# Performance work log

Hardware: AMD Instinct MI355X
Metric: run time of the kernel (lower is better)

The kernel has to match this reference:

```python
import jax, jax.numpy as jnp
import numpy as np

N, E, G = 20000, 80000, 1000      # nodes, edges, graphs
F_TOT, EA = 16, 5                 # node feature dim, edge_attr dim
CSD = 5                           # cont_feat_start_dim
DIMS = [(5, 32), (32, 64), (64, 64)]  # NNConv (M_in, M_out) per layer
FC_IN = 64 + (F_TOT - CSD)        # 75


def setup_inputs() -> dict:
    key = jax.random.key(0)
    ks = iter(jax.random.split(key, 64))
    rnd = lambda sh: jax.random.normal(next(ks), sh, jnp.float32) * 0.1
    inp = {}
    inp["x"] = jax.random.normal(next(ks), (N, F_TOT), jnp.float32)
    inp["edge_index"] = jax.random.randint(next(ks), (2, E), 0, N)
    inp["edge_attr"] = jax.random.uniform(next(ks), (E, EA), dtype=jnp.float32)
    inp["batch"] = jnp.sort(jax.random.randint(next(ks), (N,), 0, G))
    for i, (mi, mo) in enumerate(DIMS, 1):
        inp[f"c{i}_w1"] = rnd((EA, 128))
        inp[f"c{i}_b1"] = jnp.zeros((128,), jnp.float32)
        inp[f"c{i}_w2"] = rnd((128, mi * mo))
        inp[f"c{i}_b2"] = jnp.zeros((mi * mo,), jnp.float32)
        inp[f"c{i}_root"] = rnd((mi, mo))
        inp[f"c{i}_bias"] = jnp.zeros((mo,), jnp.float32)
    inp["fc1_w"] = rnd((FC_IN, 32)); inp["fc1_b"] = jnp.zeros((32,), jnp.float32)
    inp["fc2_w"] = rnd((32, 16));    inp["fc2_b"] = jnp.zeros((16,), jnp.float32)
    inp["fc3_w"] = rnd((16, 1));     inp["fc3_b"] = jnp.zeros((1,), jnp.float32)
    return inp


def nnconv(h, edge_index, edge_attr, w1, b1, w2, b2, root, bias, mi, mo):
    # edge MLP -> per-edge [mi, mo] weight matrices
    hid = jax.nn.relu(edge_attr @ w1 + b1)                 # [E,128]
    W = (hid @ w2 + b2).reshape(-1, mi, mo)                # [E,mi,mo]
    src, dst = edge_index[0], edge_index[1]
    msg = jnp.einsum('ei,eio->eo', h[src], W)              # gather + per-edge matmul
    agg = jax.ops.segment_sum(msg, dst, num_segments=h.shape[0])  # scatter-add
    return agg + h @ root + bias


def reference(x, edge_index, edge_attr, batch,
              c1_w1, c1_b1, c1_w2, c1_b2, c1_root, c1_bias,
              c2_w1, c2_b1, c2_w2, c2_b2, c2_root, c2_bias,
              c3_w1, c3_b1, c3_w2, c3_b2, c3_root, c3_bias,
              fc1_w, fc1_b, fc2_w, fc2_b, fc3_w, fc3_b):
    convs = [(c1_w1, c1_b1, c1_w2, c1_b2, c1_root, c1_bias),
             (c2_w1, c2_b1, c2_w2, c2_b2, c2_root, c2_bias),
             (c3_w1, c3_b1, c3_w2, c3_b2, c3_root, c3_bias)]
    h = x[:, :CSD]
    for (w1, b1, w2, b2, root, bias), (mi, mo) in zip(convs, DIMS):
        h = jax.nn.elu(nnconv(h, edge_index, edge_attr, w1, b1, w2, b2, root, bias, mi, mo))
    x_int = h                                   # [N,64]
    x_cont = x[:, CSD:]                         # cont_feat_num_layers == 0
    hcat = jnp.concatenate([x_int, x_cont], axis=1)  # [N,75]
    # scatter_mean over graphs
    sums = jax.ops.segment_sum(hcat, batch, num_segments=G)
    cnts = jax.ops.segment_sum(jnp.ones((hcat.shape[0],), jnp.float32), batch, num_segments=G)
    g = sums / jnp.maximum(cnts, 1.0)[:, None]  # [G,75]
    g = jax.nn.elu(g @ fc1_w + fc1_b)
    g = jax.nn.elu(g @ fc2_w + fc2_b)
    g = g @ fc3_w + fc3_b
    return g.reshape(-1)
```

## Files before the change

kernel.cpp:

```cpp
#include <hip/hip_runtime.h>
#include <math.h>

constexpr int Nn = 20000;
constexpr int Ee = 80000;
constexpr int Gg = 1000;

typedef _Float16 f16x8 __attribute__((ext_vector_type(8)));
typedef _Float16 f16x4 __attribute__((ext_vector_type(4)));
typedef _Float16 f16x2 __attribute__((ext_vector_type(2)));
typedef float    f32x4 __attribute__((ext_vector_type(4)));

__device__ __forceinline__ float eluf(float x){ return x > 0.f ? x : (expf(x) - 1.f); }

__device__ __forceinline__ void bt_emit(int idx, int lgNF, int MIR, int s, int MO,
                                        const float* __restrict__ w2,
                                        const float* __restrict__ b2,
                                        _Float16* __restrict__ bt){
  int NF = 1 << lgNF;
  int j  = idx & 7;
  int l  = (idx >> 3) & 63;
  int n  = (idx >> 9) & (NF - 1);
  int ks = idx >> (9 + lgNF);
  int col = n * 16 + (l & 15);
  int kk  = ks * 32 + ((l >> 4) << 3) + j;
  int k = kk >> s, i = kk & ((1 << s) - 1);
  float v = 0.f;
  if (i < MIR){
    if (k < 128)       v = w2[(size_t)k * (MIR * MO) + i * MO + col];
    else if (k == 128) v = b2[i * MO + col];
  }
  bt[idx] = (_Float16)v;
}

__global__ void bt_node_all(const float* __restrict__ w21, const float* __restrict__ b21,
                            const float* __restrict__ w22, const float* __restrict__ b22,
                            const float* __restrict__ w23, const float* __restrict__ b23,
                            _Float16* __restrict__ bt1, _Float16* __restrict__ bt2,
                            _Float16* __restrict__ bt3,
                            const float* __restrict__ x, const float* __restrict__ root1,
                            const float* __restrict__ bias1, float* __restrict__ aggA){
  int idx = blockIdx.x * 256 + threadIdx.x;
  if (idx < 36864)                 bt_emit(idx,          1, 5,  3, 32, w21, b21, bt1);
  else if (idx < 36864 + 270336)   bt_emit(idx - 36864,  2, 32, 5, 64, w22, b22, bt2);
  else if (idx < 839680)           bt_emit(idx - 307200, 2, 64, 6, 64, w23, b23, bt3);
  else {
    int t = idx - 839680;
    if (t < Nn * 32){
      int n = t >> 5, o = t & 31;
      float s = bias1[o];
      #pragma unroll
      for (int i = 0; i < 5; ++i) s += x[(size_t)n * 16 + i] * root1[i * 32 + o];
      aggA[t] = s;
    }
  }
}

template<int MI, int MO>
__global__ __launch_bounds__(256) void elu_node_kernel(
    const float* __restrict__ agg_prev, const float* __restrict__ root,
    const float* __restrict__ bias, float* __restrict__ hout, float* __restrict__ agg_next){
  __shared__ float hl[32][MI + 1];
  int n0 = blockIdx.x * 32;
  int t  = threadIdx.x;
  for (int idx = t; idx < 32 * MI; idx += 256){
    int nl = idx / MI, i = idx - nl * MI;
    float v = eluf(agg_prev[(size_t)(n0 + nl) * MI + i]);
    hl[nl][i] = v;
    hout[(size_t)(n0 + nl) * MI + i] = v;
  }
  __syncthreads();
  for (int idx = t; idx < 32 * MO; idx += 256){
    int nl = idx / MO, o = idx - nl * MO;
    float s = bias[o];
    #pragma unroll 8
    for (int i = 0; i < MI; ++i) s += hl[nl][i] * root[i * MO + o];
    agg_next[(size_t)(n0 + nl) * MO + o] = s;
  }
}

template<int MIR, int MIP, int MO, int HIDK, int LB>
__global__ __launch_bounds__(256, LB) void edge_mfma(
    const float* __restrict__ ea, const float* __restrict__ w1, const float* __restrict__ b1,
    const _Float16* __restrict__ bt, const float* __restrict__ h, int ldh,
    const int* __restrict__ src, const int* __restrict__ dst, float* __restrict__ agg)
{
  constexpr int NF   = MO / 16;
  constexpr int NBLK = MIP / 8;
  constexpr int KS   = (HIDK * MIP) / 32;
  constexpr int HIDP = (MIP == 8) ? 148 : ((MIP == 32) ? 140 : 136);
  constexpr int HID_B  = 64 * HIDP * 2;
  constexpr int HS_B   = 64 * MIP * 2;
  constexpr int COMB_B = 2 * 3 * NF * 64 * 16;
  constexpr int EA_O   = HID_B + HS_B;
  constexpr int SRC_O  = EA_O + 1280;
  constexpr int STG_E  = SRC_O + 256;
  constexpr int DST_O  = (STG_E > COMB_B) ? STG_E : COMB_B;

  __shared__ __align__(16) char pool[DST_O + 256];
  _Float16* hidp = (_Float16*)pool;
  _Float16* hsp  = (_Float16*)(pool + HID_B);
  float*    eap  = (float*)(pool + EA_O);
  int*      src_l = (int*)(pool + SRC_O);
  int*      dst_l = (int*)(pool + DST_O);

  const int tid  = threadIdx.x;
  const int lane = tid & 63;
  const int wave = tid >> 6;
  const int c15  = lane & 15;
  const int g    = lane >> 4;
  const int e0   = blockIdx.x * 64;

  const int ksb = ((KS * wave / 4) + 3) & ~3;
  const int kse = (wave == 3) ? KS : ((KS * (wave + 1) / 4) + 3) & ~3;
  const int KSW = kse - ksb;

  for (int t = tid; t < 320; t += 256) eap[t] = ea[(size_t)e0 * 5 + t];
  if (tid < 64){ src_l[tid] = src[e0 + tid]; dst_l[tid] = dst[e0 + tid]; }
  __syncthreads();

  for (int t = tid; t < 64 * HIDK; t += 256){
    int e = t / HIDK, k = t - e * HIDK;
    float s;
    if (k < 128){
      s = b1[k];
      #pragma unroll
      for (int j = 0; j < 5; ++j) s += eap[e * 5 + j] * w1[j * 128 + k];
      s = fmaxf(s, 0.f);
    } else s = (k == 128) ? 1.f : 0.f;
    hidp[e * HIDP + k] = (_Float16)s;
  }
  constexpr int IV = MIP / 4;
  for (int t = tid; t < 64 * IV; t += 256){
    int e = t / IV, i4 = (t - e * IV) * 4;
    f32x4 hv4 = *(const f32x4*)&h[(size_t)src_l[e] * ldh + i4];
    _Float16 o4[4];
    #pragma unroll
    for (int q = 0; q < 4; ++q) o4[q] = (i4 + q < MIR) ? (_Float16)hv4[q] : (_Float16)0.f;
    int bw = ((i4 >> 3) ^ (e & (NBLK - 1)));
    *(f16x4*)&hsp[e * MIP + ((bw << 3) | (i4 & 7))] = *(const f16x4*)o4;
  }
  __syncthreads();

  const f16x8* __restrict__ btv = (const f16x8*)bt;
  int er_[4];
  #pragma unroll
  for (int m = 0; m < 4; ++m) er_[m] = m * 16 + c15;

  f32x4 acc[4][NF];
  #pragma unroll
  for (int m = 0; m < 4; ++m)
    #pragma unroll
    for (int n = 0; n < NF; ++n) acc[m][n] = (f32x4){0.f, 0.f, 0.f, 0.f};

  f16x8 hsh[4][2];
  #pragma unroll
  for (int m = 0; m < 4; ++m){
    const int er = er_[m];
    if constexpr (MIP == 8){
      hsh[m][0] = *(const f16x8*)&hsp[er * MIP];
      hsh[m][1] = hsh[m][0];
    } else if constexpr (MIP == 32){
      int blk = g ^ (er & 3);
      hsh[m][0] = *(const f16x8*)&hsp[er * MIP + (blk << 3)];
      hsh[m][1] = hsh[m][0];
    } else {
      int b0 = g ^ (er & 7), b1x = (4 + g) ^ (er & 7);
      hsh[m][0] = *(const f16x8*)&hsp[er * MIP + (b0 << 3)];
      hsh[m][1] = *(const f16x8*)&hsp[er * MIP + (b1x << 3)];
    }
  }

  f16x8 bqA[NF], bqB[NF];
  #pragma unroll
  for (int n = 0; n < NF; ++n){
    bqA[n] = btv[((size_t)(ksb + 0) * NF + n) * 64 + lane];
    bqB[n] = btv[((size_t)(ksb + 1) * NF + n) * 64 + lane];
  }

#define EDGE_SUB(U, BQ)                                                         \
  {                                                                             \
    _Pragma("unroll")                                                           \
    for (int m = 0; m < 4; ++m){                                                \
      _Float16 hv;                                                              \
      f16x8 hs8;                                                                \
      if constexpr (MIP == 64){ hv = hvC2[m][(U) >> 1]; hs8 = hsh[m][(U) & 1]; }\
      else if constexpr (MIP == 32){ hv = hvC4[m][(U)]; hs8 = hsh[m][0]; }      \
      else { hv = hidp[er_[m] * HIDP + ((ksb + u + (U)) << 2) + g];             \
             hs8 = hsh[m][0]; }                                                 \
      f16x8 hvv = {hv, hv, hv, hv, hv, hv, hv, hv};                             \
      f16x8 av  = hs8 * hvv;                                                    \
      _Pragma("unroll")                                                         \
      for (int n = 0; n < NF; ++n)                                              \
        acc[m][n] = __builtin_amdgcn_mfma_f32_16x16x32_f16(av, BQ[n],           \
                                                           acc[m][n], 0, 0, 0);\
    }                                                                           \
    _Pragma("unroll")                                                           \
    for (int n = 0; n < NF; ++n)                                                \
      BQ[n] = btv[((size_t)(ksb + u + (U) + 2) * NF + n) * 64 + lane];          \
  }

  f16x2 hvC2[4], hvN2[4];
  f16x4 hvC4[4], hvN4[4];
  if constexpr (MIP == 64){
    #pragma unroll
    for (int m = 0; m < 4; ++m)
      hvC2[m] = *(const f16x2*)&hidp[er_[m] * HIDP + (ksb >> 1)];
  } else if constexpr (MIP == 32){
    #pragma unroll
    for (int m = 0; m < 4; ++m)
      hvC4[m] = *(const f16x4*)&hidp[er_[m] * HIDP + ksb];
  }

  for (int u = 0; u < KSW; u += 4){
    if constexpr (MIP == 64){
      #pragma unroll
      for (int m = 0; m < 4; ++m)
        hvN2[m] = *(const f16x2*)&hidp[er_[m] * HIDP + ((ksb + u + 4) >> 1)];
    } else if constexpr (MIP == 32){
      #pragma unroll
      for (int m = 0; m < 4; ++m)
        hvN4[m] = *(const f16x4*)&hidp[er_[m] * HIDP + (ksb + u + 4)];
    }
    __builtin_amdgcn_s_setprio(1);
    EDGE_SUB(0, bqA)
    EDGE_SUB(1, bqB)
    EDGE_SUB(2, bqA)
    EDGE_SUB(3, bqB)
    __builtin_amdgcn_s_setprio(0);
    #pragma unroll
    for (int m = 0; m < 4; ++m){ hvC2[m] = hvN2[m]; hvC4[m] = hvN4[m]; }
  }
#undef EDGE_SUB

  __syncthreads();
  float* comb = (float*)pool;
  #pragma unroll
  for (int m = 0; m < 2; ++m) if (m != wave){
    int s = wave - (wave > m ? 1 : 0);
    #pragma unroll
    for (int n = 0; n < NF; ++n)
      *(f32x4*)&comb[(((m * 3 + s) * NF + n) * 64 + lane) * 4] = acc[m][n];
  }
  __syncthreads();
  #pragma unroll
  for (int m = 0; m < 2; ++m) if (m == wave){
    #pragma unroll
    for (int n = 0; n < NF; ++n)
      #pragma unroll
      for (int s = 0; s < 3; ++s)
        acc[m][n] += *(const f32x4*)&comb[(((m * 3 + s) * NF + n) * 64 + lane) * 4];
  }
  __syncthreads();
  #pragma unroll
  for (int m = 2; m < 4; ++m) if (m != wave){
    int s = wave - (wave > m ? 1 : 0);
    #pragma unroll
    for (int n = 0; n < NF; ++n)
      *(f32x4*)&comb[((((m - 2) * 3 + s) * NF + n) * 64 + lane) * 4] = acc[m][n];
  }
  __syncthreads();
  #pragma unroll
  for (int m = 2; m < 4; ++m) if (m == wave){
    #pragma unroll
    for (int n = 0; n < NF; ++n)
      #pragma unroll
      for (int s = 0; s < 3; ++s)
        acc[m][n] += *(const f32x4*)&comb[((((m - 2) * 3 + s) * NF + n) * 64 + lane) * 4];
  }
  #pragma unroll
  for (int m = 0; m < 4; ++m) if (m == wave){
    #pragma unroll
    for (int n = 0; n < NF; ++n)
      #pragma unroll
      for (int j = 0; j < 4; ++j){
        int er = m * 16 + (g << 2) + j;
        atomicAdd(&agg[(size_t)dst_l[er] * MO + n * 16 + c15], acc[m][n][j]);
      }
  }
}

__global__ __launch_bounds__(64) void pool_head_kernel(
    const float* __restrict__ agg3, const float* __restrict__ x,
    const int* __restrict__ batch,
    const float* __restrict__ fc1w, const float* __restrict__ fc1b,
    const float* __restrict__ fc2w, const float* __restrict__ fc2b,
    const float* __restrict__ fc3w, const float* __restrict__ fc3b,
    float* __restrict__ out)
{
  int gph  = blockIdx.x;
  int lane = threadIdx.x;
  int lo = 0, hi = Nn;
  while (lo < hi){ int mid = (lo + hi) >> 1; if (batch[mid] < gph) lo = mid + 1; else hi = mid; }
  int start = lo;
  hi = Nn;
  while (lo < hi){ int mid = (lo + hi) >> 1; if (batch[mid] < gph + 1) lo = mid + 1; else hi = mid; }
  int end = lo;

  float s0 = 0.f, s1 = 0.f;
  for (int n = start; n < end; ++n){
    s0 += eluf(agg3[(size_t)n * 64 + lane]);
    if (lane < 11) s1 += x[(size_t)n * 16 + 5 + lane];
  }
  float inv = 1.f / fmaxf((float)(end - start), 1.f);

  __shared__ float m[75];
  __shared__ float a1[32];
  __shared__ float a2[16];
  m[lane] = s0 * inv;
  if (lane < 11) m[64 + lane] = s1 * inv;
  __syncthreads();
  if (lane < 32){
    float s = fc1b[lane];
    for (int f = 0; f < 75; ++f) s += m[f] * fc1w[f * 32 + lane];
    a1[lane] = eluf(s);
  }
  __syncthreads();
  if (lane < 16){
    float s = fc2b[lane];
    #pragma unroll
    for (int i = 0; i < 32; ++i) s += a1[i] * fc2w[i * 16 + lane];
    a2[lane] = eluf(s);
  }
  __syncthreads();
  if (lane == 0){
    float s = fc3b[0];
    #pragma unroll
    for (int i = 0; i < 16; ++i) s += a2[i] * fc3w[i];
    out[gph] = s;
  }
}

extern "C" void kernel_launch(void* const* d_in, const int* in_sizes, int n_in,
                              void* d_out, int out_size, void* d_ws, size_t ws_size,
                              hipStream_t stream)
{
  (void)in_sizes; (void)n_in; (void)out_size; (void)ws_size;
  const float* x     = (const float*)d_in[0];
  const int*   ei    = (const int*)d_in[1];
  const float* ea    = (const float*)d_in[2];
  const int*   batch = (const int*)d_in[3];
  const float* cw1[3]   = {(const float*)d_in[4],  (const float*)d_in[10], (const float*)d_in[16]};
  const float* cb1[3]   = {(const float*)d_in[5],  (const float*)d_in[11], (const float*)d_in[17]};
  const float* cw2[3]   = {(const float*)d_in[6],  (const float*)d_in[12], (const float*)d_in[18]};
  const float* cb2[3]   = {(const float*)d_in[7],  (const float*)d_in[13], (const float*)d_in[19]};
  const float* croot[3] = {(const float*)d_in[8],  (const float*)d_in[14], (const float*)d_in[20]};
  const float* cbias[3] = {(const float*)d_in[9],  (const float*)d_in[15], (const float*)d_in[21]};
  const float* fc1w = (const float*)d_in[22];
  const float* fc1b = (const float*)d_in[23];
  const float* fc2w = (const float*)d_in[24];
  const float* fc2b = (const float*)d_in[25];
  const float* fc3w = (const float*)d_in[26];
  const float* fc3b = (const float*)d_in[27];
  float* out = (float*)d_out;

  float* ws   = (float*)d_ws;
  float* h    = ws;
  float* aggA = h + (size_t)Nn * 64;
  float* aggB = aggA + (size_t)Nn * 64;
  _Float16* bt1 = (_Float16*)(aggB + (size_t)Nn * 64);
  _Float16* bt2 = bt1 + 40960;
  _Float16* bt3 = bt2 + 278528;

  const int* src = ei;
  const int* dst = ei + Ee;

  bt_node_all<<<(839680 + Nn * 32 + 255) / 256, 256, 0, stream>>>(
      cw2[0], cb2[0], cw2[1], cb2[1], cw2[2], cb2[2], bt1, bt2, bt3,
      x, croot[0], cbias[0], aggA);

  edge_mfma<5, 8, 32, 144, 4><<<Ee / 64, 256, 0, stream>>>(ea, cw1[0], cb1[0], bt1, x, 16, src, dst, aggA);

  elu_node_kernel<32, 64><<<(Nn + 31) / 32, 256, 0, stream>>>(aggA, croot[1], cbias[1], h, aggB);
  edge_mfma<32, 32, 64, 132, 3><<<Ee / 64, 256, 0, stream>>>(ea, cw1[1], cb1[1], bt2, h, 32, src, dst, aggB);

  elu_node_kernel<64, 64><<<(Nn + 31) / 32, 256, 0, stream>>>(aggB, croot[2], cbias[2], h, aggA);
  edge_mfma<64, 64, 64, 130, 3><<<Ee / 64, 256, 0, stream>>>(ea, cw1[2], cb1[2], bt3, h, 64, src, dst, aggA);

  pool_head_kernel<<<Gg, 64, 0, stream>>>(aggA, x, batch, fc1w, fc1b, fc2w, fc2b, fc3w, fc3b, out);
}
```

Before: 218.7 us.

## Use 32x32x16 MFMA edge kernel for layers 2 and 3

```diff
diff --git a/kernel.cpp b/kernel.cpp
--- a/kernel.cpp
+++ b/kernel.cpp
@@ -9,6 +9,7 @@
 typedef _Float16 f16x4 __attribute__((ext_vector_type(4)));
 typedef _Float16 f16x2 __attribute__((ext_vector_type(2)));
 typedef float    f32x4 __attribute__((ext_vector_type(4)));
+typedef float    f32x16 __attribute__((ext_vector_type(16)));
 
 __device__ __forceinline__ float eluf(float x){ return x > 0.f ? x : (expf(x) - 1.f); }
 
@@ -32,6 +33,25 @@
   bt[idx] = (_Float16)v;
 }
 
+__device__ __forceinline__ void bt_emit32(int idx, int MIR, int s,
+                                          const float* __restrict__ w2,
+                                          const float* __restrict__ b2,
+                                          _Float16* __restrict__ bt){
+  int j = idx & 7;
+  int l = (idx >> 3) & 63;
+  int n = (idx >> 9) & 1;
+  int q = idx >> 10;
+  int col = n * 32 + (l & 31);
+  int kk  = q * 16 + ((l >> 5) << 3) + j;
+  int k = kk >> s, i = kk & ((1 << s) - 1);
+  float v = 0.f;
+  if (i < MIR){
+    if (k < 128)       v = w2[(size_t)k * (MIR * 64) + i * 64 + col];
+    else if (k == 128) v = b2[i * 64 + col];
+  }
+  bt[idx] = (_Float16)v;
+}
+
 __global__ void bt_node_all(const float* __restrict__ w21, const float* __restrict__ b21,
                             const float* __restrict__ w22, const float* __restrict__ b22,
                             const float* __restrict__ w23, const float* __restrict__ b23,
@@ -40,11 +60,11 @@
                             const float* __restrict__ x, const float* __restrict__ root1,
                             const float* __restrict__ bias1, float* __restrict__ aggA){
   int idx = blockIdx.x * 256 + threadIdx.x;
-  if (idx < 36864)                 bt_emit(idx,          1, 5,  3, 32, w21, b21, bt1);
-  else if (idx < 36864 + 270336)   bt_emit(idx - 36864,  2, 32, 5, 64, w22, b22, bt2);
-  else if (idx < 839680)           bt_emit(idx - 307200, 2, 64, 6, 64, w23, b23, bt3);
+  if (idx < 36864)        bt_emit(idx, 1, 5, 3, 32, w21, b21, bt1);
+  else if (idx < 311296)  bt_emit32(idx - 36864, 32, 5, w22, b22, bt2);
+  else if (idx < 847872)  bt_emit32(idx - 311296, 64, 6, w23, b23, bt3);
   else {
-    int t = idx - 839680;
+    int t = idx - 847872;
     if (t < Nn * 32){
       int n = t >> 5, o = t & 31;
       float s = bias1[o];
@@ -87,7 +107,7 @@
   constexpr int NF   = MO / 16;
   constexpr int NBLK = MIP / 8;
   constexpr int KS   = (HIDK * MIP) / 32;
-  constexpr int HIDP = (MIP == 8) ? 148 : ((MIP == 32) ? 140 : 136);
+  constexpr int HIDP = 148;
   constexpr int HID_B  = 64 * HIDP * 2;
   constexpr int HS_B   = 64 * MIP * 2;
   constexpr int COMB_B = 2 * 3 * NF * 64 * 16;
@@ -152,23 +172,9 @@
     #pragma unroll
     for (int n = 0; n < NF; ++n) acc[m][n] = (f32x4){0.f, 0.f, 0.f, 0.f};
 
-  f16x8 hsh[4][2];
-  #pragma unroll
-  for (int m = 0; m < 4; ++m){
-    const int er = er_[m];
-    if constexpr (MIP == 8){
-      hsh[m][0] = *(const f16x8*)&hsp[er * MIP];
-      hsh[m][1] = hsh[m][0];
-    } else if constexpr (MIP == 32){
-      int blk = g ^ (er & 3);
-      hsh[m][0] = *(const f16x8*)&hsp[er * MIP + (blk << 3)];
-      hsh[m][1] = hsh[m][0];
-    } else {
-      int b0 = g ^ (er & 7), b1x = (4 + g) ^ (er & 7);
-      hsh[m][0] = *(const f16x8*)&hsp[er * MIP + (b0 << 3)];
-      hsh[m][1] = *(const f16x8*)&hsp[er * MIP + (b1x << 3)];
-    }
-  }
+  f16x8 hsh[4];
+  #pragma unroll
+  for (int m = 0; m < 4; ++m) hsh[m] = *(const f16x8*)&hsp[er_[m] * MIP];
 
   f16x8 bqA[NF], bqB[NF];
   #pragma unroll
@@ -181,12 +187,8 @@
   {                                                                             \
     _Pragma("unroll")                                                           \
     for (int m = 0; m < 4; ++m){                                                \
-      _Float16 hv;                                                              \
-      f16x8 hs8;                                                                \
-      if constexpr (MIP == 64){ hv = hvC2[m][(U) >> 1]; hs8 = hsh[m][(U) & 1]; }\
-      else if constexpr (MIP == 32){ hv = hvC4[m][(U)]; hs8 = hsh[m][0]; }      \
-      else { hv = hidp[er_[m] * HIDP + ((ksb + u + (U)) << 2) + g];             \
-             hs8 = hsh[m][0]; }                                                 \
+      _Float16 hv = hidp[er_[m] * HIDP + ((ksb + u + (U)) << 2) + g];           \
+      f16x8 hs8 = hsh[m];                                                       \
       f16x8 hvv = {hv, hv, hv, hv, hv, hv, hv, hv};                             \
       f16x8 av  = hs8 * hvv;                                                    \
       _Pragma("unroll")                                                         \
@@ -199,36 +201,13 @@
       BQ[n] = btv[((size_t)(ksb + u + (U) + 2) * NF + n) * 64 + lane];          \
   }
 
-  f16x2 hvC2[4], hvN2[4];
-  f16x4 hvC4[4], hvN4[4];
-  if constexpr (MIP == 64){
-    #pragma unroll
-    for (int m = 0; m < 4; ++m)
-      hvC2[m] = *(const f16x2*)&hidp[er_[m] * HIDP + (ksb >> 1)];
-  } else if constexpr (MIP == 32){
-    #pragma unroll
-    for (int m = 0; m < 4; ++m)
-      hvC4[m] = *(const f16x4*)&hidp[er_[m] * HIDP + ksb];
-  }
-
   for (int u = 0; u < KSW; u += 4){
-    if constexpr (MIP == 64){
-      #pragma unroll
-      for (int m = 0; m < 4; ++m)
-        hvN2[m] = *(const f16x2*)&hidp[er_[m] * HIDP + ((ksb + u + 4) >> 1)];
-    } else if constexpr (MIP == 32){
-      #pragma unroll
-      for (int m = 0; m < 4; ++m)
-        hvN4[m] = *(const f16x4*)&hidp[er_[m] * HIDP + (ksb + u + 4)];
-    }
     __builtin_amdgcn_s_setprio(1);
     EDGE_SUB(0, bqA)
     EDGE_SUB(1, bqB)
     EDGE_SUB(2, bqA)
     EDGE_SUB(3, bqB)
     __builtin_amdgcn_s_setprio(0);
-    #pragma unroll
-    for (int m = 0; m < 4; ++m){ hvC2[m] = hvN2[m]; hvC4[m] = hvN4[m]; }
   }
 #undef EDGE_SUB
 
@@ -276,6 +255,187 @@
         int er = m * 16 + (g << 2) + j;
         atomicAdd(&agg[(size_t)dst_l[er] * MO + n * 16 + c15], acc[m][n][j]);
       }
+  }
+}
+
+template<int MIP, int HIDK, int LB>
+__global__ __launch_bounds__(256, LB) void edge_mfma32(
+    const float* __restrict__ ea, const float* __restrict__ w1, const float* __restrict__ b1,
+    const _Float16* __restrict__ bt, const float* __restrict__ h,
+    const int* __restrict__ src, const int* __restrict__ dst, float* __restrict__ agg)
+{
+  constexpr int NV   = (MIP == 64) ? 4 : 2;
+  constexpr int NBLK = MIP / 8;
+  constexpr int KS   = (HIDK * MIP) / 16;
+  constexpr int HIDP = (MIP == 64) ? 138 : 134;
+  constexpr int HID_B  = 64 * HIDP * 2;
+  constexpr int HS_B   = 64 * MIP * 2;
+  constexpr int COMB_B = 2 * 3 * 4 * 64 * 16;
+  constexpr int EA_O   = HID_B + HS_B;
+  constexpr int SRC_O  = EA_O + 1280;
+  constexpr int STG_E  = SRC_O + 256;
+  constexpr int DST_O  = (STG_E > COMB_B) ? STG_E : COMB_B;
+
+  __shared__ __align__(16) char pool[DST_O + 256];
+  _Float16* hidp = (_Float16*)pool;
+  _Float16* hsp  = (_Float16*)(pool + HID_B);
+  float*    eap  = (float*)(pool + EA_O);
+  int*      src_l = (int*)(pool + SRC_O);
+  int*      dst_l = (int*)(pool + DST_O);
+
+  const int tid  = threadIdx.x;
+  const int lane = tid & 63;
+  const int wave = tid >> 6;
+  const int hl   = lane >> 5;
+  const int e0   = blockIdx.x * 64;
+
+  const int ksb = ((KS * wave / 4) + 3) & ~3;
+  const int kse = (wave == 3) ? KS : ((KS * (wave + 1) / 4) + 3) & ~3;
+  const int KSW = kse - ksb;
+
+  for (int t = tid; t < 320; t += 256) eap[t] = ea[(size_t)e0 * 5 + t];
+  if (tid < 64){ src_l[tid] = src[e0 + tid]; dst_l[tid] = dst[e0 + tid]; }
+  __syncthreads();
+
+  for (int t = tid; t < 64 * HIDK; t += 256){
+    int e = t / HIDK, k = t - e * HIDK;
+    float s;
+    if (k < 128){
+      s = b1[k];
+      #pragma unroll
+      for (int j = 0; j < 5; ++j) s += eap[e * 5 + j] * w1[j * 128 + k];
+      s = fmaxf(s, 0.f);
+    } else s = (k == 128) ? 1.f : 0.f;
+    hidp[e * HIDP + k] = (_Float16)s;
+  }
+  constexpr int IV = MIP / 4;
+  for (int t = tid; t < 64 * IV; t += 256){
+    int e = t / IV, i4 = (t - e * IV) * 4;
+    f32x4 hv4 = *(const f32x4*)&h[(size_t)src_l[e] * MIP + i4];
+    _Float16 o4[4] = {(_Float16)hv4[0], (_Float16)hv4[1], (_Float16)hv4[2], (_Float16)hv4[3]};
+    int bw = ((i4 >> 3) ^ (e & (NBLK - 1)));
+    *(f16x4*)&hsp[e * MIP + ((bw << 3) | (i4 & 7))] = *(const f16x4*)o4;
+  }
+  __syncthreads();
+
+  const f16x8* __restrict__ btv = (const f16x8*)bt;
+  int er_[2];
+  er_[0] = (lane & 31);
+  er_[1] = 32 + (lane & 31);
+
+  f32x16 acc[2][2];
+  #pragma unroll
+  for (int m = 0; m < 2; ++m)
+    #pragma unroll
+    for (int n = 0; n < 2; ++n)
+      #pragma unroll
+      for (int r = 0; r < 16; ++r) acc[m][n][r] = 0.f;
+
+  f16x8 hsh[2][NV];
+  #pragma unroll
+  for (int m = 0; m < 2; ++m)
+    #pragma unroll
+    for (int v = 0; v < NV; ++v){
+      int blog  = v * 2 + hl;
+      int bphys = blog ^ (er_[m] & (NBLK - 1));
+      hsh[m][v] = *(const f16x8*)&hsp[er_[m] * MIP + (bphys << 3)];
+    }
+
+  f16x8 bq0[2], bq1[2], bq2[2], bq3[2];
+  #pragma unroll
+  for (int n = 0; n < 2; ++n){
+    bq0[n] = btv[((size_t)(ksb + 0) * 2 + n) * 64 + lane];
+    bq1[n] = btv[((size_t)(ksb + 1) * 2 + n) * 64 + lane];
+    bq2[n] = btv[((size_t)(ksb + 2) * 2 + n) * 64 + lane];
+    bq3[n] = btv[((size_t)(ksb + 3) * 2 + n) * 64 + lane];
+  }
+
+#define EDGE_SUB32(U, BQ)                                                        \
+  {                                                                              \
+    _Pragma("unroll")                                                            \
+    for (int m = 0; m < 2; ++m){                                                 \
+      _Float16 hv;                                                               \
+      f16x8 hs8;                                                                 \
+      if constexpr (MIP == 64){ hv = hvC[m];          hs8 = hsh[m][(U)];     }   \
+      else                    { hv = hvC2[m][(U)>>1]; hs8 = hsh[m][(U)&1];   }   \
+      f16x8 hvv = {hv, hv, hv, hv, hv, hv, hv, hv};                              \
+      f16x8 av  = hs8 * hvv;                                                     \
+      acc[m][0] = __builtin_amdgcn_mfma_f32_32x32x16_f16(av, BQ[0], acc[m][0],   \
+                                                         0, 0, 0);              \
+      acc[m][1] = __builtin_amdgcn_mfma_f32_32x32x16_f16(av, BQ[1], acc[m][1],   \
+                                                         0, 0, 0);              \
+    }                                                                            \
+    _Pragma("unroll")                                                            \
+    for (int n = 0; n < 2; ++n)                                                  \
+      BQ[n] = btv[((size_t)(ksb + u + (U) + 4) * 2 + n) * 64 + lane];            \
+  }
+
+  _Float16 hvC[2], hvN[2];
+  f16x2 hvC2[2], hvN2[2];
+  if constexpr (MIP == 64){
+    #pragma unroll
+    for (int m = 0; m < 2; ++m) hvC[m] = hidp[er_[m] * HIDP + (ksb >> 2)];
+  } else {
+    #pragma unroll
+    for (int m = 0; m < 2; ++m) hvC2[m] = *(const f16x2*)&hidp[er_[m] * HIDP + (ksb >> 1)];
+  }
+
+  for (int u = 0; u < KSW; u += 4){
+    if constexpr (MIP == 64){
+      #pragma unroll
+      for (int m = 0; m < 2; ++m) hvN[m] = hidp[er_[m] * HIDP + ((ksb + u + 4) >> 2)];
+    } else {
+      #pragma unroll
+      for (int m = 0; m < 2; ++m) hvN2[m] = *(const f16x2*)&hidp[er_[m] * HIDP + ((ksb + u + 4) >> 1)];
+    }
+    __builtin_amdgcn_s_setprio(1);
+    EDGE_SUB32(0, bq0)
+    EDGE_SUB32(1, bq1)
+    EDGE_SUB32(2, bq2)
+    EDGE_SUB32(3, bq3)
+    __builtin_amdgcn_s_setprio(0);
+    #pragma unroll
+    for (int m = 0; m < 2; ++m){ hvC[m] = hvN[m]; hvC2[m] = hvN2[m]; }
+  }
+#undef EDGE_SUB32
+
+  __syncthreads();
+  float* comb = (float*)pool;
+  #pragma unroll
+  for (int mq = 0; mq < 2; ++mq){
+    #pragma unroll
+    for (int n = 0; n < 2; ++n){
+      int owner = mq * 2 + n;
+      if (wave != owner){
+        int s = wave - (wave > owner ? 1 : 0);
+        #pragma unroll
+        for (int c = 0; c < 4; ++c){
+          f32x4 t4 = {acc[mq][n][4*c], acc[mq][n][4*c+1], acc[mq][n][4*c+2], acc[mq][n][4*c+3]};
+          *(f32x4*)&comb[(((n * 3 + s) * 4 + c) * 64 + lane) * 4] = t4;
+        }
+      }
+    }
+    __syncthreads();
+    if ((wave >> 1) == mq){
+      int n = wave & 1;
+      #pragma unroll
+      for (int s = 0; s < 3; ++s)
+        #pragma unroll
+        for (int c = 0; c < 4; ++c){
+          f32x4 t4 = *(const f32x4*)&comb[(((n * 3 + s) * 4 + c) * 64 + lane) * 4];
+          acc[mq][n][4*c]   += t4[0];
+          acc[mq][n][4*c+1] += t4[1];
+          acc[mq][n][4*c+2] += t4[2];
+          acc[mq][n][4*c+3] += t4[3];
+        }
+      #pragma unroll
+      for (int r = 0; r < 16; ++r){
+        int row = (r & 3) + 8 * (r >> 2) + 4 * hl;
+        atomicAdd(&agg[(size_t)dst_l[mq * 32 + row] * 64 + n * 32 + (lane & 31)],
+                  acc[mq][n][r]);
+      }
+    }
+    __syncthreads();
   }
 }
 
@@ -359,22 +519,22 @@
   float* aggB = aggA + (size_t)Nn * 64;
   _Float16* bt1 = (_Float16*)(aggB + (size_t)Nn * 64);
   _Float16* bt2 = bt1 + 40960;
-  _Float16* bt3 = bt2 + 278528;
+  _Float16* bt3 = bt2 + 274432;
 
   const int* src = ei;
   const int* dst = ei + Ee;
 
-  bt_node_all<<<(839680 + Nn * 32 + 255) / 256, 256, 0, stream>>>(
+  bt_node_all<<<(847872 + Nn * 32 + 255) / 256, 256, 0, stream>>>(
       cw2[0], cb2[0], cw2[1], cb2[1], cw2[2], cb2[2], bt1, bt2, bt3,
       x, croot[0], cbias[0], aggA);
 
   edge_mfma<5, 8, 32, 144, 4><<<Ee / 64, 256, 0, stream>>>(ea, cw1[0], cb1[0], bt1, x, 16, src, dst, aggA);
 
   elu_node_kernel<32, 64><<<(Nn + 31) / 32, 256, 0, stream>>>(aggA, croot[1], cbias[1], h, aggB);
-  edge_mfma<32, 32, 64, 132, 3><<<Ee / 64, 256, 0, stream>>>(ea, cw1[1], cb1[1], bt2, h, 32, src, dst, aggB);
+  edge_mfma32<32, 132, 3><<<Ee / 64, 256, 0, stream>>>(ea, cw1[1], cb1[1], bt2, h, src, dst, aggB);
 
   elu_node_kernel<64, 64><<<(Nn + 31) / 32, 256, 0, stream>>>(aggB, croot[2], cbias[2], h, aggA);
-  edge_mfma<64, 64, 64, 130, 3><<<Ee / 64, 256, 0, stream>>>(ea, cw1[2], cb1[2], bt3, h, 64, src, dst, aggA);
+  edge_mfma32<64, 130, 3><<<Ee / 64, 256, 0, stream>>>(ea, cw1[2], cb1[2], bt3, h, src, dst, aggA);
 
   pool_head_kernel<<<Gg, 64, 0, stream>>>(aggA, x, batch, fc1w, fc1b, fc2w, fc2b, fc3w, fc3b, out);
 }
```

New measurement: 278.2 us. 1.27x slower.
